# Kernel optimization log

Measured on AMD Instinct MI355X. Metric: run time of the kernel, lower is better.

Reference implementation:

```python
import jax, jax.numpy as jnp
import numpy as np

DIM = 2048
NUM_HEADS = 32
NUM_KV_HEADS = 8
HEAD_DIM = DIM // NUM_HEADS  # 64
GROUPS = NUM_HEADS // NUM_KV_HEADS  # 4
B, L = 2, 2048


def setup_inputs() -> dict:
    key = jax.random.key(0)
    ks = jax.random.split(key, 7)
    s = 0.02
    return {
        "x": jax.random.normal(ks[0], (B, L, DIM), dtype=jnp.float32),
        "Wq": jax.random.normal(ks[1], (DIM, DIM), dtype=jnp.float32) * s,
        "bq": jax.random.normal(ks[2], (DIM,), dtype=jnp.float32) * s,
        "Wkv": jax.random.normal(ks[3], (2 * NUM_KV_HEADS * HEAD_DIM, DIM), dtype=jnp.float32) * s,
        "bkv": jax.random.normal(ks[4], (2 * NUM_KV_HEADS * HEAD_DIM,), dtype=jnp.float32) * s,
        "Wo": jax.random.normal(ks[5], (DIM, DIM), dtype=jnp.float32) * s,
        "bo": jax.random.normal(ks[6], (DIM,), dtype=jnp.float32) * s,
        "causal": 1,
    }


def reference(x, Wq, bq, Wkv, bkv, Wo, bo, causal):
    b, l, d = x.shape
    # Q projection -> (B, H, L, hd)
    q = (x @ Wq.T + bq).reshape(b, l, NUM_HEADS, HEAD_DIM).transpose(0, 2, 1, 3)
    # KV projection -> (B, L, 2, Hkv, hd)
    kv = (x @ Wkv.T + bkv).reshape(b, l, 2, NUM_KV_HEADS, HEAD_DIM)
    k = kv[:, :, 0].transpose(0, 2, 1, 3)  # (B, Hkv, L, hd)
    v = kv[:, :, 1].transpose(0, 2, 1, 3)
    # GQA expand: head h attends kv head h // GROUPS (consecutive repeat)
    k = jnp.repeat(k, GROUPS, axis=1)  # (B, H, L, hd)
    v = jnp.repeat(v, GROUPS, axis=1)
    scale = 1.0 / np.sqrt(HEAD_DIM).astype(np.float32)
    scores = jnp.einsum("bhqd,bhkd->bhqk", q, k) * scale
    if causal:
        mask = jnp.tril(jnp.ones((l, l), dtype=bool))
        scores = jnp.where(mask, scores, jnp.finfo(scores.dtype).min)
    attn = jax.nn.softmax(scores, axis=-1)
    out = jnp.einsum("bhqk,bhkd->bhqd", attn, v)  # (B, H, L, hd)
    out = out.transpose(0, 2, 1, 3).reshape(b, l, d)
    return out @ Wo.T + bo
```

## Files before the change

kernel.cpp:

```cpp
#include <hip/hip_runtime.h>
#include <hip/hip_bf16.h>
#include <stdint.h>

#define DIM 2048
#define SEQ 2048
#define BATCH 2
#define NHEADS 32
#define NKV 8
#define HD 64
#define MROWS (BATCH*SEQ)
#define KVDIM (2*NKV*HD)
#define NQKV (DIM + KVDIM)

typedef __bf16 bf16_t;
typedef __bf16 bf16x8 __attribute__((ext_vector_type(8)));
typedef __bf16 bf16x4 __attribute__((ext_vector_type(4)));
typedef float  f32x4  __attribute__((ext_vector_type(4)));

#define GLD16(gsrc, ldst) __builtin_amdgcn_global_load_lds( \
    (__attribute__((address_space(1))) void*)(gsrc), \
    (__attribute__((address_space(3))) void*)(ldst), 16, 0, 0)

#define NX4 (MROWS*DIM/4)
#define NQ4 (DIM*DIM/4)
#define NK4 (KVDIM*DIM/4)
__global__ __launch_bounds__(256) void cast3_kernel(
    const float* __restrict__ x, const float* __restrict__ wq,
    const float* __restrict__ wkv, bf16_t* __restrict__ xb,
    bf16_t* __restrict__ wqkv) {
    int i = blockIdx.x * blockDim.x + threadIdx.x;
    const float4* src; bf16x4* dst; int j;
    if (i < NX4)            { src = (const float4*)x;   dst = (bf16x4*)xb;   j = i; }
    else if (i < NX4+NQ4)   { src = (const float4*)wq;  dst = (bf16x4*)wqkv; j = i - NX4; }
    else if (i < NX4+NQ4+NK4){ src = (const float4*)wkv; dst = (bf16x4*)wqkv + NQ4; j = i - NX4 - NQ4; }
    else return;
    float4 f = src[j];
    bf16x4 o;
    o[0] = (bf16_t)f.x; o[1] = (bf16_t)f.y; o[2] = (bf16_t)f.z; o[3] = (bf16_t)f.w;
    dst[j] = o;
}

__global__ __launch_bounds__(256) void cast_kernel(const float* __restrict__ in,
                                                   bf16_t* __restrict__ out, int n4) {
    int i = blockIdx.x * blockDim.x + threadIdx.x;
    if (i >= n4) return;
    float4 f = ((const float4*)in)[i];
    bf16x4 o;
    o[0] = (bf16_t)f.x; o[1] = (bf16_t)f.y; o[2] = (bf16_t)f.z; o[3] = (bf16_t)f.w;
    ((bf16x4*)out)[i] = o;
}

template<int MODE>
__global__ __launch_bounds__(256) void gemm_bt(
    const bf16_t* __restrict__ A, const bf16_t* __restrict__ W,
    const float* __restrict__ bias, const float* __restrict__ bias2,
    void* __restrict__ Cp, bf16_t* __restrict__ Kbp, bf16_t* __restrict__ VTp,
    int M, int N, int K)
{
    __shared__ bf16_t As[128*32];
    __shared__ bf16_t Bs[128*32];
    const int brow = blockIdx.y * 128;
    const int bcol = blockIdx.x * 128;
    const int tid  = threadIdx.x;
    const int lane = tid & 63;
    const int w    = tid >> 6;
    const int wr   = w >> 1, wc = w & 1;
    const int l16  = lane & 15, l4 = lane >> 4;

    f32x4 acc[4][4];
#pragma unroll
    for (int m = 0; m < 4; m++)
#pragma unroll
        for (int n = 0; n < 4; n++) acc[m][n] = (f32x4){0.f, 0.f, 0.f, 0.f};

    const int r  = tid >> 2;
    const int c8 = (tid & 3) << 3;
    const bf16_t* ga = A + (size_t)(brow + r) * K + c8;
    const bf16_t* gb = W + (size_t)(bcol + r) * K + c8;
    const int wbase = w * 512;

    const int ard = (wr*64 + l16)*32 + l4*8;
    const int brd = (wc*64 + l16)*32 + l4*8;

    for (int kt = 0; kt < K; kt += 32) {
        __syncthreads();
        GLD16(ga + kt,                 &As[wbase]);
        GLD16(ga + (size_t)64*K + kt,  &As[2048 + wbase]);
        GLD16(gb + kt,                 &Bs[wbase]);
        GLD16(gb + (size_t)64*K + kt,  &Bs[2048 + wbase]);
        __syncthreads();
        bf16x8 af[4], bfr[4];
#pragma unroll
        for (int m = 0; m < 4; m++) af[m]  = *(const bf16x8*)&As[ard + m*16*32];
#pragma unroll
        for (int n = 0; n < 4; n++) bfr[n] = *(const bf16x8*)&Bs[brd + n*16*32];
#pragma unroll
        for (int m = 0; m < 4; m++)
#pragma unroll
            for (int n = 0; n < 4; n++)
                acc[m][n] = __builtin_amdgcn_mfma_f32_16x16x32_bf16(af[m], bfr[n], acc[m][n], 0, 0, 0);
    }

#pragma unroll
    for (int m = 0; m < 4; m++) {
        int row0 = brow + wr*64 + m*16 + l4*4;
#pragma unroll
        for (int n = 0; n < 4; n++) {
            int col = bcol + wc*64 + n*16 + l16;
            if (MODE == 0) {
                float bv = bias[col];
#pragma unroll
                for (int rr = 0; rr < 4; rr++)
                    ((float*)Cp)[(size_t)(row0+rr)*DIM + col] = acc[m][n][rr] + bv;
            } else {
                if (col < DIM) {
                    float bv = bias[col];
#pragma unroll
                    for (int rr = 0; rr < 4; rr++)
                        ((bf16_t*)Cp)[(size_t)(row0+rr)*DIM + col] =
                            (bf16_t)((acc[m][n][rr] + bv) * 0.125f);
                } else if (col < DIM + 512) {
                    int kc = col - DIM;
                    float bv = bias2[kc];
#pragma unroll
                    for (int rr = 0; rr < 4; rr++)
                        Kbp[(size_t)(row0+rr)*512 + kc] = (bf16_t)(acc[m][n][rr] + bv);
                } else {
                    int dall = col - DIM - 512;
                    int kvh = dall >> 6, d = dall & 63;
                    int b = row0 >> 11, s0 = row0 & 2047;
                    float bv = bias2[col - DIM];
                    bf16x4 pv;
#pragma unroll
                    for (int rr = 0; rr < 4; rr++) pv[rr] = (bf16_t)(acc[m][n][rr] + bv);
                    *(bf16x4*)&VTp[((size_t)((b*NKV + kvh)*HD + d))*SEQ + s0] = pv;
                }
            }
        }
    }
}

__global__ __launch_bounds__(256, 2) void attn_kernel(
    const bf16_t* __restrict__ Qm,
    const bf16_t* __restrict__ Kb,
    const bf16_t* __restrict__ VT,
    bf16_t* __restrict__ Am,
    const int* __restrict__ causalp)
{
    __shared__ bf16_t Ks[2][4096];
    __shared__ bf16_t Vs[2][4096];
    __shared__ char   Pl[4*4096];

    const int B     = blockIdx.x;
    const int xcd   = B & 7;
    const int s_    = B >> 3;
    const int group = xcd + 8*(s_ >> 5);
    const int inner = s_ & 31;
    const int b     = group >> 3;
    const int kvh   = group & 7;
    const int h     = kvh*4 + (inner >> 3);
    const int px    = inner & 7;

    const int tid  = threadIdx.x;
    const int lane = tid & 63;
    const int w    = tid >> 6;
    const int l16  = lane & 15, l4 = lane >> 4;
    const int causal = *causalp;

    const int srow  = tid >> 3;
    const int selem = 8 * ((tid & 7) ^ (srow & 7));
    const bf16_t* ksrc = Kb + (size_t)(b*SEQ + srow)*512 + kvh*64 + selem;
    const bf16_t* vsrc = VT + ((size_t)((b*NKV + kvh)*HD) + srow)*SEQ + selem;
    const int d0 = w*512, d1 = 2048 + w*512;

    char* plw = Pl + w*4096;

    int koff[4][2];
#pragma unroll
    for (int n = 0; n < 4; n++)
#pragma unroll
        for (int kk = 0; kk < 2; kk++)
            koff[n][kk] = (n*16 + l16)*64 + ((kk*32 + l4*8) ^ ((l16 & 7)*8));

    int cur = 0;
    auto STAGE = [&](int kt, int buf) {
        GLD16(ksrc + (size_t)(kt*64)*512,      &Ks[buf][d0]);
        GLD16(ksrc + (size_t)(kt*64+32)*512,   &Ks[buf][d1]);
        GLD16(vsrc + kt*64,                    &Vs[buf][d0]);
        GLD16(vsrc + (size_t)32*SEQ + kt*64,   &Vs[buf][d1]);
    };

    STAGE(0, 0);

    for (int half = 0; half < 2; half++) {
        const int t    = causal ? (half ? 15 - px : px) : (px + half*8);
        const int rowb = t*128;
        const int nkt  = causal ? 2*t + 2 : (SEQ/64);

        bf16x8 qf[2][2];
#pragma unroll
        for (int m = 0; m < 2; m++) {
            const bf16_t* qbase = Qm + (size_t)(b*SEQ + rowb + w*32 + m*16 + l16)*DIM + h*HD + l4*8;
            qf[m][0] = *(const bf16x8*)qbase;
            qf[m][1] = *(const bf16x8*)(qbase + 32);
        }

        f32x4 o[2][4];
#pragma unroll
        for (int m = 0; m < 2; m++)
#pragma unroll
            for (int n = 0; n < 4; n++) o[m][n] = (f32x4){0.f,0.f,0.f,0.f};
        float srun[2][4];
#pragma unroll
        for (int m = 0; m < 2; m++)
#pragma unroll
            for (int rr = 0; rr < 4; rr++) srun[m][rr] = 0.f;

        for (int kt = 0; kt < nkt; kt++) {
            __syncthreads();
            if (kt + 1 < nkt)            STAGE(kt + 1, cur ^ 1);
            else if (half == 0)          STAGE(0, cur ^ 1);

            f32x4 s[2][4];
#pragma unroll
            for (int m = 0; m < 2; m++)
#pragma unroll
                for (int n = 0; n < 4; n++) s[m][n] = (f32x4){0.f,0.f,0.f,0.f};
            __builtin_amdgcn_s_setprio(1);
#pragma unroll
            for (int n = 0; n < 4; n++)
#pragma unroll
                for (int kk = 0; kk < 2; kk++) {
                    bf16x8 kf = *(const bf16x8*)&Ks[cur][koff[n][kk]];
#pragma unroll
                    for (int m = 0; m < 2; m++)
                        s[m][n] = __builtin_amdgcn_mfma_f32_16x16x32_bf16(qf[m][kk], kf, s[m][n], 0, 0, 0);
                }
            __builtin_amdgcn_s_setprio(0);

            if (causal && kt*64 + 63 > rowb + w*32) {
#pragma unroll
                for (int m = 0; m < 2; m++)
#pragma unroll
                    for (int n = 0; n < 4; n++) {
                        int col = kt*64 + n*16 + l16;
#pragma unroll
                        for (int rr = 0; rr < 4; rr++) {
                            int row = rowb + w*32 + m*16 + l4*4 + rr;
                            if (col > row) s[m][n][rr] = -1e30f;
                        }
                    }
            }

#pragma unroll
            for (int m = 0; m < 2; m++)
#pragma unroll
                for (int n = 0; n < 4; n++)
#pragma unroll
                    for (int rr = 0; rr < 4; rr++) {
                        float p = __expf(s[m][n][rr]);
                        srun[m][rr] += p;
                        int row = m*16 + l4*4 + rr;
                        int byo = row*128 + (((n*16 + l16)*2) ^ ((((row >> 3) ^ row) & 7) << 4));
                        *(bf16_t*)(plw + byo) = (bf16_t)p;
                    }

            bf16x8 pa[2][2];
#pragma unroll
            for (int m = 0; m < 2; m++)
#pragma unroll
                for (int kk = 0; kk < 2; kk++) {
                    int row = m*16 + l16;
                    int byo = row*128 + ((kk*64 + l4*16) ^ ((((row >> 3) ^ row) & 7) << 4));
                    pa[m][kk] = *(const bf16x8*)(plw + byo);
                }
            __builtin_amdgcn_s_setprio(1);
#pragma unroll
            for (int n = 0; n < 4; n++)
#pragma unroll
                for (int kk = 0; kk < 2; kk++) {
                    bf16x8 vf = *(const bf16x8*)&Vs[cur][koff[n][kk]];
#pragma unroll
                    for (int m = 0; m < 2; m++)
                        o[m][n] = __builtin_amdgcn_mfma_f32_16x16x32_bf16(pa[m][kk], vf, o[m][n], 0, 0, 0);
                }
            __builtin_amdgcn_s_setprio(0);
            cur ^= 1;
        }

#pragma unroll
        for (int m = 0; m < 2; m++)
#pragma unroll
            for (int rr = 0; rr < 4; rr++) {
                float ts = srun[m][rr];
                ts += __shfl_xor(ts, 1);
                ts += __shfl_xor(ts, 2);
                ts += __shfl_xor(ts, 4);
                ts += __shfl_xor(ts, 8);
                srun[m][rr] = ts;
            }

#pragma unroll
        for (int m = 0; m < 2; m++)
#pragma unroll
            for (int n = 0; n < 4; n++) {
                int col = h*HD + n*16 + l16;
#pragma unroll
                for (int rr = 0; rr < 4; rr++) {
                    int row = b*SEQ + rowb + w*32 + m*16 + l4*4 + rr;
                    Am[(size_t)row*DIM + col] = (bf16_t)(o[m][n][rr] / srun[m][rr]);
                }
            }
    }
}

extern "C" void kernel_launch(void* const* d_in, const int* in_sizes, int n_in,
                              void* d_out, int out_size, void* d_ws, size_t ws_size,
                              hipStream_t stream) {
    const float* x    = (const float*)d_in[0];
    const float* Wq   = (const float*)d_in[1];
    const float* bq   = (const float*)d_in[2];
    const float* Wkv  = (const float*)d_in[3];
    const float* bkv  = (const float*)d_in[4];
    const float* Wo   = (const float*)d_in[5];
    const float* bo   = (const float*)d_in[6];
    const int* causal = (const int*)d_in[7];

    char* ws = (char*)d_ws;
    bf16_t* xb   = (bf16_t*)(ws);
    bf16_t* wqkv = (bf16_t*)(ws + (16u << 20));
    bf16_t* Qb   = (bf16_t*)(ws + (30u << 20));
    bf16_t* Kb   = (bf16_t*)(ws + (46u << 20));
    bf16_t* VT   = (bf16_t*)(ws + (50u << 20));
    bf16_t* Ab   = xb;

    cast3_kernel<<<(NX4+NQ4+NK4 + 255)/256, 256, 0, stream>>>(x, Wq, Wkv, xb, wqkv);
    gemm_bt<3><<<dim3(NQKV/128, MROWS/128), 256, 0, stream>>>(
        xb, wqkv, bq, bkv, Qb, Kb, VT, MROWS, NQKV, DIM);
    cast_kernel<<<(NQ4 + 255)/256, 256, 0, stream>>>(Wo, wqkv, NQ4);
    attn_kernel<<<dim3(512), 256, 0, stream>>>(Qb, Kb, VT, Ab, causal);
    gemm_bt<0><<<dim3(DIM/128, MROWS/128), 256, 0, stream>>>(
        Ab, wqkv, bo, nullptr, d_out, nullptr, nullptr, MROWS, DIM, DIM);
}
```

Before: 205.7 us.

## Double GEMM K-tile to 64 with XOR-swizzled LDS and merge Wo cast

```diff
diff --git a/kernel.cpp b/kernel.cpp
--- a/kernel.cpp
+++ b/kernel.cpp
@@ -24,30 +24,22 @@
 #define NX4 (MROWS*DIM/4)
 #define NQ4 (DIM*DIM/4)
 #define NK4 (KVDIM*DIM/4)
-__global__ __launch_bounds__(256) void cast3_kernel(
+#define NO4 (DIM*DIM/4)
+__global__ __launch_bounds__(256) void cast4_kernel(
     const float* __restrict__ x, const float* __restrict__ wq,
-    const float* __restrict__ wkv, bf16_t* __restrict__ xb,
-    bf16_t* __restrict__ wqkv) {
+    const float* __restrict__ wkv, const float* __restrict__ wo,
+    bf16_t* __restrict__ xb, bf16_t* __restrict__ wqkv, bf16_t* __restrict__ wob) {
     int i = blockIdx.x * blockDim.x + threadIdx.x;
     const float4* src; bf16x4* dst; int j;
-    if (i < NX4)            { src = (const float4*)x;   dst = (bf16x4*)xb;   j = i; }
-    else if (i < NX4+NQ4)   { src = (const float4*)wq;  dst = (bf16x4*)wqkv; j = i - NX4; }
-    else if (i < NX4+NQ4+NK4){ src = (const float4*)wkv; dst = (bf16x4*)wqkv + NQ4; j = i - NX4 - NQ4; }
+    if (i < NX4)                   { src = (const float4*)x;   dst = (bf16x4*)xb;        j = i; }
+    else if (i < NX4+NQ4)          { src = (const float4*)wq;  dst = (bf16x4*)wqkv;      j = i - NX4; }
+    else if (i < NX4+NQ4+NK4)      { src = (const float4*)wkv; dst = (bf16x4*)wqkv + NQ4; j = i - NX4 - NQ4; }
+    else if (i < NX4+NQ4+NK4+NO4)  { src = (const float4*)wo;  dst = (bf16x4*)wob;       j = i - NX4 - NQ4 - NK4; }
     else return;
     float4 f = src[j];
     bf16x4 o;
     o[0] = (bf16_t)f.x; o[1] = (bf16_t)f.y; o[2] = (bf16_t)f.z; o[3] = (bf16_t)f.w;
     dst[j] = o;
-}
-
-__global__ __launch_bounds__(256) void cast_kernel(const float* __restrict__ in,
-                                                   bf16_t* __restrict__ out, int n4) {
-    int i = blockIdx.x * blockDim.x + threadIdx.x;
-    if (i >= n4) return;
-    float4 f = ((const float4*)in)[i];
-    bf16x4 o;
-    o[0] = (bf16_t)f.x; o[1] = (bf16_t)f.y; o[2] = (bf16_t)f.z; o[3] = (bf16_t)f.w;
-    ((bf16x4*)out)[i] = o;
 }
 
 template<int MODE>
@@ -57,8 +49,8 @@
     void* __restrict__ Cp, bf16_t* __restrict__ Kbp, bf16_t* __restrict__ VTp,
     int M, int N, int K)
 {
-    __shared__ bf16_t As[128*32];
-    __shared__ bf16_t Bs[128*32];
+    __shared__ bf16_t As[128*64];
+    __shared__ bf16_t Bs[128*64];
     const int brow = blockIdx.y * 128;
     const int bcol = blockIdx.x * 128;
     const int tid  = threadIdx.x;
@@ -73,32 +65,45 @@
 #pragma unroll
         for (int n = 0; n < 4; n++) acc[m][n] = (f32x4){0.f, 0.f, 0.f, 0.f};
 
-    const int r  = tid >> 2;
-    const int c8 = (tid & 3) << 3;
-    const bf16_t* ga = A + (size_t)(brow + r) * K + c8;
-    const bf16_t* gb = W + (size_t)(bcol + r) * K + c8;
+    const int r2 = tid >> 3;
+    const int selem = 8 * ((tid & 7) ^ (r2 & 7));
+    const bf16_t* ga = A + (size_t)(brow + r2) * K + selem;
+    const bf16_t* gb = W + (size_t)(bcol + r2) * K + selem;
     const int wbase = w * 512;
 
-    const int ard = (wr*64 + l16)*32 + l4*8;
-    const int brd = (wc*64 + l16)*32 + l4*8;
-
-    for (int kt = 0; kt < K; kt += 32) {
+    const int xk = (l16 & 7) * 8;
+    int aoff[4][2], boff[4][2];
+#pragma unroll
+    for (int m = 0; m < 4; m++)
+#pragma unroll
+        for (int kk = 0; kk < 2; kk++) {
+            aoff[m][kk] = (wr*64 + m*16 + l16)*64 + ((kk*32 + l4*8) ^ xk);
+            boff[m][kk] = (wc*64 + m*16 + l16)*64 + ((kk*32 + l4*8) ^ xk);
+        }
+
+    for (int kt = 0; kt < K; kt += 64) {
         __syncthreads();
-        GLD16(ga + kt,                 &As[wbase]);
-        GLD16(ga + (size_t)64*K + kt,  &As[2048 + wbase]);
-        GLD16(gb + kt,                 &Bs[wbase]);
-        GLD16(gb + (size_t)64*K + kt,  &Bs[2048 + wbase]);
+#pragma unroll
+        for (int j = 0; j < 4; j++) {
+            GLD16(ga + (size_t)(j*32)*K + kt, &As[j*2048 + wbase]);
+            GLD16(gb + (size_t)(j*32)*K + kt, &Bs[j*2048 + wbase]);
+        }
         __syncthreads();
-        bf16x8 af[4], bfr[4];
-#pragma unroll
-        for (int m = 0; m < 4; m++) af[m]  = *(const bf16x8*)&As[ard + m*16*32];
-#pragma unroll
-        for (int n = 0; n < 4; n++) bfr[n] = *(const bf16x8*)&Bs[brd + n*16*32];
+        bf16x8 af[4][2], bfr[4][2];
 #pragma unroll
         for (int m = 0; m < 4; m++)
 #pragma unroll
+            for (int kk = 0; kk < 2; kk++) {
+                af[m][kk]  = *(const bf16x8*)&As[aoff[m][kk]];
+                bfr[m][kk] = *(const bf16x8*)&Bs[boff[m][kk]];
+            }
+#pragma unroll
+        for (int m = 0; m < 4; m++)
+#pragma unroll
             for (int n = 0; n < 4; n++)
-                acc[m][n] = __builtin_amdgcn_mfma_f32_16x16x32_bf16(af[m], bfr[n], acc[m][n], 0, 0, 0);
+#pragma unroll
+                for (int kk = 0; kk < 2; kk++)
+                    acc[m][n] = __builtin_amdgcn_mfma_f32_16x16x32_bf16(af[m][kk], bfr[n][kk], acc[m][n], 0, 0, 0);
     }
 
 #pragma unroll
@@ -332,13 +337,14 @@
     bf16_t* Qb   = (bf16_t*)(ws + (30u << 20));
     bf16_t* Kb   = (bf16_t*)(ws + (46u << 20));
     bf16_t* VT   = (bf16_t*)(ws + (50u << 20));
+    bf16_t* wob  = (bf16_t*)(ws + (54u << 20));
     bf16_t* Ab   = xb;
 
-    cast3_kernel<<<(NX4+NQ4+NK4 + 255)/256, 256, 0, stream>>>(x, Wq, Wkv, xb, wqkv);
+    cast4_kernel<<<(NX4+NQ4+NK4+NO4 + 255)/256, 256, 0, stream>>>(
+        x, Wq, Wkv, Wo, xb, wqkv, wob);
     gemm_bt<3><<<dim3(NQKV/128, MROWS/128), 256, 0, stream>>>(
         xb, wqkv, bq, bkv, Qb, Kb, VT, MROWS, NQKV, DIM);
-    cast_kernel<<<(NQ4 + 255)/256, 256, 0, stream>>>(Wo, wqkv, NQ4);
     attn_kernel<<<dim3(512), 256, 0, stream>>>(Qb, Kb, VT, Ab, causal);
     gemm_bt<0><<<dim3(DIM/128, MROWS/128), 256, 0, stream>>>(
-        Ab, wqkv, bo, nullptr, d_out, nullptr, nullptr, MROWS, DIM, DIM);
+        Ab, wob, bo, nullptr, d_out, nullptr, nullptr, MROWS, DIM, DIM);
 }
```

Measured after the change: 184.8 us, median of 3. 1.11x faster.
